# Optimization experiments

Hardware: AMD Instinct MI355X
Metric: run time of the kernel (lower is better)

## Reference

```python
import jax, jax.numpy as jnp
import numpy as np

MAX_POS = 512  # hardcoded max_pos_emb in the module
LN_EPS = 1e-5


def setup_inputs() -> dict:
    key = jax.random.key(0)
    ks = jax.random.split(key, 6)
    bs, n, d = 16, 4000, 1024
    h, dh = 8, 128
    inner = h * dh
    return {
        "x": jax.random.normal(ks[0], (bs, n, d), jnp.float32),
        "ln_w": jnp.ones((d,), jnp.float32),
        "ln_b": jnp.zeros((d,), jnp.float32),
        "Wq": (jax.random.normal(ks[1], (inner, d), jnp.float32) * 0.02),
        "Wkv": (jax.random.normal(ks[2], (2 * inner, d), jnp.float32) * 0.02),
        "Wo": (jax.random.normal(ks[3], (d, inner), jnp.float32) * 0.02),
        "bo": jnp.zeros((d,), jnp.float32),
        "rel_emb": (jax.random.normal(ks[4], (2 * MAX_POS + 1, dh), jnp.float32) * 0.02),
        "context_size": 256,
    }


def reference(x, ln_w, ln_b, Wq, Wkv, Wo, bo, rel_emb, context_size):
    bs, n, d = x.shape
    dh = rel_emb.shape[1]
    h = Wq.shape[0] // dh
    scale = dh ** -0.5
    cs = int(context_size)
    nb = -(-n // cs)          # ceil(n / cs)
    nr = n % cs

    # pre_norm (LayerNorm)
    mu = jnp.mean(x, axis=-1, keepdims=True)
    var = jnp.var(x, axis=-1, keepdims=True)
    xn = (x - mu) * jax.lax.rsqrt(var + LN_EPS) * ln_w + ln_b
    if nr > 0:
        xn = jnp.pad(xn, ((0, 0), (0, cs - nr), (0, 0)))

    q = xn @ Wq.T                    # (bs, nb*cs, h*dh)
    k, v = jnp.split(xn @ Wkv.T, 2, axis=-1)

    def blk(t):  # -> (bs, nb, h, cs, dh)
        return t.reshape(bs, nb, cs, h, dh).transpose(0, 1, 3, 2, 4)

    q, k, v = blk(q), blk(k), blk(v)

    # relative position bias, computed as a GEMM instead of broadcast-mul-sum
    seq = jnp.arange(cs)
    dist = jnp.clip(seq[:, None] - seq[None, :], -cs, cs) + MAX_POS
    rel = rel_emb[dist]                                     # (cs, cs, dh)
    pos_attn = jnp.einsum('bnhid,ijd->bnhij', q, rel) * scale

    if nr > 0:
        m = np.ones((cs, cs), dtype=bool)
        m[:nr, :nr] = False
        neg = -jnp.finfo(pos_attn.dtype).max
        pos_attn = pos_attn.at[:, -1].set(
            jnp.where(jnp.asarray(m), neg, pos_attn[:, -1]))

    # SDPA with additive mask: softmax(q k^T * scale + pos_attn) v
    scores = jnp.einsum('bnhid,bnhjd->bnhij', q, k) * scale + pos_attn
    attn = jax.nn.softmax(scores, axis=-1)
    out = jnp.einsum('bnhij,bnhjd->bnhid', attn, v)         # (bs, nb, h, cs, dh)

    out = out.transpose(0, 1, 3, 2, 4).reshape(bs, nb * cs, h * dh)[:, :n]
    return out @ Wo.T + bo  # dropout is identity in eval
```

## Files before the change

kernel.cpp:

```cpp
#include <hip/hip_runtime.h>

typedef __bf16 bf16;
typedef __bf16 bf16x8 __attribute__((ext_vector_type(8)));
typedef float f32x4 __attribute__((ext_vector_type(4)));

#define MFMA16(A,B,C) __builtin_amdgcn_mfma_f32_16x16x32_bf16(A,B,C,0,0,0)
#define SCALE 0.08838834764831843f
#define NEGBIG (-1e30f)

#define AS1(p) ((__attribute__((address_space(1))) void*)(p))
#define AS3(p) ((__attribute__((address_space(3))) void*)(p))

#define BAR() do { asm volatile("" ::: "memory"); __builtin_amdgcn_s_barrier(); asm volatile("" ::: "memory"); } while (0)

__global__ void cvt_bf16(const float* __restrict__ src, bf16* __restrict__ dst, int n) {
    int i = (blockIdx.x * 256 + threadIdx.x) * 4;
    if (i < n) {
        float4 v = *(const float4*)(src + i);
        dst[i + 0] = (bf16)v.x; dst[i + 1] = (bf16)v.y;
        dst[i + 2] = (bf16)v.z; dst[i + 3] = (bf16)v.w;
    }
}

__global__ __launch_bounds__(256) void ln_kernel(const float* __restrict__ x,
                                                 const float* __restrict__ w,
                                                 const float* __restrict__ b,
                                                 bf16* __restrict__ xn) {
    int row = blockIdx.x;
    int bb = row >> 12, p = row & 4095;
    int t = threadIdx.x;
    bf16* out = xn + ((size_t)row << 10);
    if (p >= 4000) {
        uint2 z; z.x = 0u; z.y = 0u;
        *(uint2*)(out + t * 4) = z;
        return;
    }
    float4 v = *(const float4*)(x + (((size_t)bb * 4000 + p) << 10) + t * 4);
    float s = v.x + v.y + v.z + v.w;
    float s2 = v.x * v.x + v.y * v.y + v.z * v.z + v.w * v.w;
#pragma unroll
    for (int m = 1; m < 64; m <<= 1) { s += __shfl_xor(s, m); s2 += __shfl_xor(s2, m); }
    __shared__ float red[8];
    int wv = t >> 6, l = t & 63;
    if (l == 0) { red[wv] = s; red[4 + wv] = s2; }
    __syncthreads();
    s = red[0] + red[1] + red[2] + red[3];
    s2 = red[4] + red[5] + red[6] + red[7];
    float mu = s * (1.f / 1024.f);
    float var = s2 * (1.f / 1024.f) - mu * mu;
    float inv = rsqrtf(var + 1e-5f);
    float4 wv4 = *(const float4*)(w + t * 4);
    float4 bv4 = *(const float4*)(b + t * 4);
    union { bf16 h[4]; uint2 u; } o;
    o.h[0] = (bf16)((v.x - mu) * inv * wv4.x + bv4.x);
    o.h[1] = (bf16)((v.y - mu) * inv * wv4.y + bv4.y);
    o.h[2] = (bf16)((v.z - mu) * inv * wv4.z + bv4.z);
    o.h[3] = (bf16)((v.w - mu) * inv * wv4.w + bv4.w);
    *(uint2*)(out + t * 4) = o.u;
}


__device__ __forceinline__ void stage_half(const bf16* __restrict__ src, int srow, int K,
                                           int kofs, bf16* ldsb, int w, int l) {
#pragma unroll
    for (int r = 0; r < 2; ++r) {
        int rh = (r * 8 + w) * 8 + (l >> 3);
        int chunk = (l & 7) ^ (rh & 7);
        __builtin_amdgcn_global_load_lds(AS1(src + (size_t)(srow + rh) * K + kofs + chunk * 8),
                                         AS3(ldsb + (r * 8 + w) * 512), 16, 0, 0);
    }
}

__device__ __forceinline__ bf16x8 fragLD(const bf16* base, int row, int ks, int lk) {
    int ch = ((ks * 4 + lk) ^ (row & 7)) * 8;
    return *(const bf16x8*)(base + row * 64 + ch);
}

#define RDA(AF, base, mofs) \
    _Pragma("unroll") for (int m = 0; m < 4; ++m) \
    _Pragma("unroll") for (int ks = 0; ks < 2; ++ks) \
        AF[m][ks] = fragLD(base, rA + (mofs + m) * 16 + lrow, ks, lk);

#define RDB2(nb, base) \
    _Pragma("unroll") for (int n = 0; n < 2; ++n) \
    _Pragma("unroll") for (int ks = 0; ks < 2; ++ks) \
        bfr[(nb) + n][ks] = fragLD(base, rB + ((nb) + n) * 16 + lrow, ks, lk);

#define MM(mb, AF, nb) do { \
    __builtin_amdgcn_s_setprio(1); \
    _Pragma("unroll") for (int m = 0; m < 4; ++m) \
    _Pragma("unroll") for (int n = 0; n < 2; ++n) \
    _Pragma("unroll") for (int ks = 0; ks < 2; ++ks) \
        acc[(mb) + m][(nb) + n] = MFMA16(AF[m][ks], bfr[(nb) + n][ks], acc[(mb) + m][(nb) + n]); \
    __builtin_amdgcn_s_setprio(0); } while (0)

template <int EPI>
__global__ __launch_bounds__(512, 2) void gemm256(const bf16* __restrict__ A,
                                                  const bf16* __restrict__ B,
                                                  bf16* __restrict__ C,
                                                  float* __restrict__ Cf,
                                                  const float* __restrict__ bias,
                                                  int M, int N, int K) {
    __shared__ __align__(16) bf16 LA[2 * 16384];
    __shared__ __align__(16) bf16 LB[2 * 16384];
    const int t = threadIdx.x;
    const int w = t >> 6, l = t & 63;
    const int lrow = l & 15, lk = l >> 4;
    const int wrM = w >> 2, wn = w & 3;
    const int rA = wrM * 128, rB = wn * 64;

    const int nwg = gridDim.x, cpx = nwg >> 3;
    const int swz = ((int)blockIdx.x & 7) * cpx + ((int)blockIdx.x >> 3);
    const int nbk = N >> 8;
    const int m0 = (swz / nbk) * 256;
    const int n0 = (swz % nbk) * 256;

    bf16* LA0 = LA;          bf16* LB0 = LB;
    bf16* LA1 = LA + 16384;  bf16* LB1 = LB + 16384;

    f32x4 acc[8][4] = {};
    bf16x8 afL[4][2], afH[4][2], bfr[4][2];

    const int NT = K >> 6, NI = K >> 7;

    stage_half(B, n0,       K, 0,  LB0,        w, l);
    stage_half(B, n0 + 128, K, 0,  LB0 + 8192, w, l);
    stage_half(A, m0,       K, 0,  LA0,        w, l);
    stage_half(A, m0 + 128, K, 0,  LA0 + 8192, w, l);
    stage_half(B, n0,       K, 64, LB1,        w, l);
    stage_half(B, n0 + 128, K, 64, LB1 + 8192, w, l);
    stage_half(A, m0,       K, 64, LA1,        w, l);
    asm volatile("s_waitcnt vmcnt(6)" ::: "memory");
    BAR();

    for (int i = 0; i < NI; ++i) {
        const int kS1 = (2 * i + 1) << 6;
        const int t2 = 2 * i + 2, t3 = 2 * i + 3;
        const int kS2 = ((t2 < NT) ? t2 : NT - 1) << 6;
        const int kS3 = ((t3 < NT) ? t3 : NT - 1) << 6;

        RDA(afL, LA0, 0);
        if (wn < 2) { RDB2(0, LB0); RDB2(2, LB0); } else { RDB2(0, LB0); }
        stage_half(A, m0 + 128, K, kS1, LA1 + 8192, w, l);
        BAR();
        MM(0, afL, 0);
        BAR();
        if (wn >= 2) { RDB2(2, LB0); }
        stage_half(B, n0, K, kS2, LB0, w, l);
        BAR();
        MM(0, afL, 2);
        BAR();
        RDA(afH, LA0, 4);
        stage_half(B, n0 + 128, K, kS2, LB0 + 8192, w, l);
        BAR();
        MM(4, afH, 0);
        BAR();
        stage_half(A, m0, K, kS2, LA0, w, l);
        BAR();
        MM(4, afH, 2);
        asm volatile("s_waitcnt vmcnt(6)" ::: "memory");
        BAR();
        RDA(afL, LA1, 0);
        if (wn < 2) { RDB2(0, LB1); RDB2(2, LB1); } else { RDB2(0, LB1); }
        stage_half(A, m0 + 128, K, kS2, LA0 + 8192, w, l);
        BAR();
        MM(0, afL, 0);
        BAR();
        if (wn >= 2) { RDB2(2, LB1); }
        stage_half(B, n0, K, kS3, LB1, w, l);
        BAR();
        MM(0, afL, 2);
        BAR();
        RDA(afH, LA1, 4);
        stage_half(B, n0 + 128, K, kS3, LB1 + 8192, w, l);
        BAR();
        MM(4, afH, 0);
        BAR();
        stage_half(A, m0, K, kS3, LA1, w, l);
        BAR();
        MM(4, afH, 2);
        asm volatile("s_waitcnt vmcnt(6)" ::: "memory");
        BAR();
    }

    asm volatile("s_waitcnt vmcnt(0)" ::: "memory");

    if (EPI == 0) {
#pragma unroll
        for (int m = 0; m < 8; ++m)
#pragma unroll
            for (int r = 0; r < 4; ++r) {
                size_t row = (size_t)(m0 + rA + m * 16 + lk * 4 + r);
                bf16* dst = C + row * N + n0 + rB;
#pragma unroll
                for (int n = 0; n < 4; ++n) dst[n * 16 + lrow] = (bf16)acc[m][n][r];
            }
    } else {
#pragma unroll
        for (int m = 0; m < 8; ++m)
#pragma unroll
            for (int r = 0; r < 4; ++r) {
                int row = m0 + rA + m * 16 + lk * 4 + r;
                int p = row & 4095, bb2 = row >> 12;
                if (p < 4000) {
                    float* dst = Cf + ((size_t)bb2 * 4000 + p) * 1024 + n0 + rB;
#pragma unroll
                    for (int n = 0; n < 4; ++n)
                        dst[n * 16 + lrow] = acc[m][n][r] + bias[n0 + rB + n * 16 + lrow];
                }
            }
    }
}

__global__ __launch_bounds__(512, 1) void attn_kernel(const bf16* __restrict__ qkv,
                                                      const bf16* __restrict__ relw,
                                                      bf16* __restrict__ ao) {
    int bb = blockIdx.x;
    int h = bb & 7, blkn = (bb >> 3) & 15, b = bb >> 7;
    const int t = threadIdx.x, w = t >> 6, l = t & 63, lrow = l & 15, lk = l >> 4;
    size_t qrow0 = (size_t)(b * 4096 + blkn * 256);
    __shared__ __align__(16) bf16 Vt[128 * 264];
    __shared__ __align__(16) bf16 Ps[8][16 * 72];

    const int i0 = w * 32;
    const bool last = (blkn == 15);
    const bf16* kbase = qkv + qrow0 * 3072 + 1024 + h * 128;

#pragma unroll
    for (int q = 0; q < 8; ++q) {
        int idx = q * 512 + t;
        int row = idx >> 4, c8 = idx & 15;
        bf16x8 vv = *(const bf16x8*)(qkv + (qrow0 + row) * 3072 + 2048 + h * 128 + c8 * 8);
        int jsw = row ^ ((c8 & 7) << 3);
#pragma unroll
        for (int e = 0; e < 8; ++e)
            Vt[(c8 * 8 + e) * 264 + jsw] = vv[e];
    }

    bf16x8 aq[2][4];
#pragma unroll
    for (int mt = 0; mt < 2; ++mt)
#pragma unroll
        for (int ks = 0; ks < 4; ++ks)
            aq[mt][ks] = *(const bf16x8*)(qkv + (qrow0 + i0 + mt * 16 + lrow) * 3072 +
                                          h * 128 + ks * 32 + lk * 8);

    f32x4 o[2][8] = {};
    float mrun[2][4], lrun[2][4];
#pragma unroll
    for (int mt = 0; mt < 2; ++mt)
#pragma unroll
        for (int r = 0; r < 4; ++r) { mrun[mt][r] = NEGBIG; lrun[mt][r] = 0.f; }

    __syncthreads();

    const int g0 = lk * 4 + 63 - lrow;
    bf16* ps = &Ps[w][0];

    for (int jt = 0; jt < 4; ++jt) {
        f32x4 s[2][4] = {};
        __builtin_amdgcn_s_setprio(1);
#pragma unroll
        for (int nt = 0; nt < 4; ++nt)
#pragma unroll
            for (int ks = 0; ks < 4; ++ks) {
                bf16x8 bk = *(const bf16x8*)(kbase +
                                (size_t)(jt * 64 + nt * 16 + lrow) * 3072 +
                                ks * 32 + lk * 8);
                s[0][nt] = MFMA16(aq[0][ks], bk, s[0][nt]);
                s[1][nt] = MFMA16(aq[1][ks], bk, s[1][nt]);
            }
        __builtin_amdgcn_s_setprio(0);

        const int cbase = i0 - jt * 64 + 192;
        f32x4 wacc[2][6] = {};
        __builtin_amdgcn_s_setprio(1);
#pragma unroll
        for (int ks = 0; ks < 4; ++ks)
#pragma unroll
            for (int ct = 0; ct < 6; ++ct) {
                bf16x8 br = *(const bf16x8*)(relw + (size_t)(cbase + ct * 16 + lrow) * 128 +
                                             ks * 32 + lk * 8);
                wacc[0][ct] = MFMA16(aq[0][ks], br, wacc[0][ct]);
                wacc[1][ct] = MFMA16(aq[1][ks], br, wacc[1][ct]);
            }
        __builtin_amdgcn_s_setprio(0);

#pragma unroll
        for (int mt = 0; mt < 2; ++mt)
#pragma unroll
            for (int r = 0; r < 4; ++r) {
                const int Kb = g0 + mt * 16 + r;
                const int dst = ((l & 48) | (Kb & 15)) << 2;
                unsigned pk[3];
#pragma unroll
                for (int P = 0; P < 3; ++P) {
                    unsigned lo = (unsigned)__builtin_bit_cast(unsigned short,
                                        (bf16)wacc[mt][2 * P][r]);
                    unsigned hi = (unsigned)__builtin_bit_cast(unsigned short,
                                        (bf16)wacc[mt][2 * P + 1][r]);
                    pk[P] = (unsigned)__builtin_amdgcn_ds_permute(dst, (int)((hi << 16) | lo));
                }
#pragma unroll
                for (int nt = 0; nt < 4; ++nt) {
                    int bcc = Kb - 16 * nt;
                    unsigned rec = (bcc < 32) ? pk[0] : (bcc < 64) ? pk[1] : pk[2];
                    unsigned b16v = ((bcc >> 4) & 1) ? (rec >> 16) : (rec & 0xffffu);
                    float wvf = __builtin_bit_cast(float, b16v << 16);
                    float xv = (s[mt][nt][r] + wvf) * SCALE;
                    if (last && (i0 + mt * 16 + lk * 4 + r >= 160 ||
                                 jt * 64 + nt * 16 + lrow >= 160))
                        xv = NEGBIG;
                    s[mt][nt][r] = xv;
                }
            }

#pragma unroll
        for (int mt = 0; mt < 2; ++mt)
#pragma unroll
            for (int r = 0; r < 4; ++r) {
                float mx = fmaxf(fmaxf(s[mt][0][r], s[mt][1][r]),
                                 fmaxf(s[mt][2][r], s[mt][3][r]));
#pragma unroll
                for (int d = 1; d < 16; d <<= 1) mx = fmaxf(mx, __shfl_xor(mx, d));
                float mold = mrun[mt][r];
                float mn = fmaxf(mold, mx);
                float corr = __expf(mold - mn);
                mrun[mt][r] = mn;
                float rs = 0.f;
#pragma unroll
                for (int nt = 0; nt < 4; ++nt) {
                    float e = __expf(s[mt][nt][r] - mn);
                    s[mt][nt][r] = e; rs += e;
                }
#pragma unroll
                for (int d = 1; d < 16; d <<= 1) rs += __shfl_xor(rs, d);
                lrun[mt][r] = lrun[mt][r] * corr + rs;
#pragma unroll
                for (int dt = 0; dt < 8; ++dt) o[mt][dt][r] *= corr;
            }

#pragma unroll
        for (int mt = 0; mt < 2; ++mt) {
#pragma unroll
            for (int nt = 0; nt < 4; ++nt)
#pragma unroll
                for (int r = 0; r < 4; ++r)
                    ps[(lk * 4 + r) * 72 + nt * 16 + lrow] = (bf16)s[mt][nt][r];
            __builtin_amdgcn_s_setprio(1);
#pragma unroll
            for (int pks = 0; pks < 2; ++pks) {
                bf16x8 ap = *(const bf16x8*)&ps[lrow * 72 + pks * 32 + lk * 8];
#pragma unroll
                for (int dt = 0; dt < 8; ++dt) {
                    int d = dt * 16 + lrow;
                    int jch = ((jt * 64 + pks * 32 + lk * 8) >> 3) ^ ((d >> 3) & 7);
                    bf16x8 bv = *(const bf16x8*)&Vt[d * 264 + (jch << 3)];
                    o[mt][dt] = MFMA16(ap, bv, o[mt][dt]);
                }
            }
            __builtin_amdgcn_s_setprio(0);
        }
    }

#pragma unroll
    for (int mt = 0; mt < 2; ++mt)
#pragma unroll
        for (int r = 0; r < 4; ++r) {
            float inv = 1.0f / lrun[mt][r];
            size_t arow = qrow0 + i0 + mt * 16 + lk * 4 + r;
            bf16* dst = ao + arow * 1024 + h * 128;
#pragma unroll
            for (int dt = 0; dt < 8; ++dt)
                dst[dt * 16 + lrow] = (bf16)(o[mt][dt][r] * inv);
        }
}

extern "C" void kernel_launch(void* const* d_in, const int* in_sizes, int n_in,
                              void* d_out, int out_size, void* d_ws, size_t ws_size,
                              hipStream_t stream) {
    const float* x   = (const float*)d_in[0];
    const float* lnw = (const float*)d_in[1];
    const float* lnb = (const float*)d_in[2];
    const float* Wq  = (const float*)d_in[3];
    const float* Wkv = (const float*)d_in[4];
    const float* Wo  = (const float*)d_in[5];
    const float* bo  = (const float*)d_in[6];
    const float* rel = (const float*)d_in[7];

    const size_t OFF_XN   = 0;
    const size_t OFF_QKV  = OFF_XN + 134217728ULL;
    const size_t OFF_WCAT = OFF_QKV + 402653184ULL;
    const size_t OFF_WO   = OFF_WCAT + 6291456ULL;
    const size_t OFF_RELW = OFF_WO + 2097152ULL;
    const size_t NEED     = OFF_RELW + 131072ULL;
    if (ws_size < NEED) return;

    char* ws = (char*)d_ws;
    bf16* xn   = (bf16*)(ws + OFF_XN);
    bf16* qkv  = (bf16*)(ws + OFF_QKV);
    bf16* wcat = (bf16*)(ws + OFF_WCAT);
    bf16* wo   = (bf16*)(ws + OFF_WO);
    bf16* relw = (bf16*)(ws + OFF_RELW);
    bf16* ao   = xn;
    float* out = (float*)d_out;

    cvt_bf16<<<1024, 256, 0, stream>>>(Wq, wcat, 1048576);
    cvt_bf16<<<2048, 256, 0, stream>>>(Wkv, wcat + 1048576, 2097152);
    cvt_bf16<<<1024, 256, 0, stream>>>(Wo, wo, 1048576);
    cvt_bf16<<<64, 256, 0, stream>>>(rel + 257 * 128, relw, 65536);
    ln_kernel<<<65536, 256, 0, stream>>>(x, lnw, lnb, xn);
    gemm256<0><<<3072, 512, 0, stream>>>(xn, wcat, qkv, nullptr, nullptr, 65536, 3072, 1024);
    attn_kernel<<<2048, 512, 0, stream>>>(qkv, relw, ao);
    gemm256<1><<<1024, 512, 0, stream>>>(ao, wo, nullptr, out, bo, 65536, 1024, 1024);
}
```

Measured before the change: 1.143 ms.

## Restructure attention to 16 waves with LDS-staged K/V tiles per key block

The attention kernel now uses 1024 threads with each wave owning 16 query rows instead of 32. K is staged in LDS 64 rows at a time rather than read per wave from global memory, and V is staged in a smaller per-tile transposed buffer. The next tile is loaded into registers before a barrier pair. The relative-position GEMM drops from 6 to 5 column tiles per wave because each wave covers fewer rows. This cuts redundant global K reads and LDS footprint but adds two block-wide barriers per key tile, and it halves the per-wave reuse of each B fragment.

```diff
diff --git a/kernel.cpp b/kernel.cpp
--- a/kernel.cpp
+++ b/kernel.cpp
@@ -212,45 +212,41 @@
     }
 }
 
-__global__ __launch_bounds__(512, 1) void attn_kernel(const bf16* __restrict__ qkv,
-                                                      const bf16* __restrict__ relw,
-                                                      bf16* __restrict__ ao) {
+__global__ __launch_bounds__(1024, 1) void attn_kernel(const bf16* __restrict__ qkv,
+                                                       const bf16* __restrict__ relw,
+                                                       bf16* __restrict__ ao) {
     int bb = blockIdx.x;
     int h = bb & 7, blkn = (bb >> 3) & 15, b = bb >> 7;
     const int t = threadIdx.x, w = t >> 6, l = t & 63, lrow = l & 15, lk = l >> 4;
     size_t qrow0 = (size_t)(b * 4096 + blkn * 256);
-    __shared__ __align__(16) bf16 Vt[128 * 264];
-    __shared__ __align__(16) bf16 Ps[8][16 * 72];
-
-    const int i0 = w * 32;
+    __shared__ __align__(16) bf16 Ks[64 * 136];
+    __shared__ __align__(16) bf16 Vt[128 * 72];
+    __shared__ __align__(16) bf16 Ps[16][16 * 72];
+
+    const int i0 = w * 16;
     const bool last = (blkn == 15);
-    const bf16* kbase = qkv + qrow0 * 3072 + 1024 + h * 128;
-
-#pragma unroll
-    for (int q = 0; q < 8; ++q) {
-        int idx = q * 512 + t;
-        int row = idx >> 4, c8 = idx & 15;
-        bf16x8 vv = *(const bf16x8*)(qkv + (qrow0 + row) * 3072 + 2048 + h * 128 + c8 * 8);
-        int jsw = row ^ ((c8 & 7) << 3);
+    const int srow = t >> 4, sc8 = t & 15;
+
+    {
+        bf16x8 kv = *(const bf16x8*)(qkv + (qrow0 + srow) * 3072 + 1024 + h * 128 + sc8 * 8);
+        *(bf16x8*)&Ks[srow * 136 + sc8 * 8] = kv;
+        bf16x8 vv = *(const bf16x8*)(qkv + (qrow0 + srow) * 3072 + 2048 + h * 128 + sc8 * 8);
+        int jsw = srow ^ ((sc8 & 7) << 3);
 #pragma unroll
         for (int e = 0; e < 8; ++e)
-            Vt[(c8 * 8 + e) * 264 + jsw] = vv[e];
-    }
-
-    bf16x8 aq[2][4];
-#pragma unroll
-    for (int mt = 0; mt < 2; ++mt)
-#pragma unroll
-        for (int ks = 0; ks < 4; ++ks)
-            aq[mt][ks] = *(const bf16x8*)(qkv + (qrow0 + i0 + mt * 16 + lrow) * 3072 +
-                                          h * 128 + ks * 32 + lk * 8);
-
-    f32x4 o[2][8] = {};
-    float mrun[2][4], lrun[2][4];
-#pragma unroll
-    for (int mt = 0; mt < 2; ++mt)
-#pragma unroll
-        for (int r = 0; r < 4; ++r) { mrun[mt][r] = NEGBIG; lrun[mt][r] = 0.f; }
+            Vt[(sc8 * 8 + e) * 72 + jsw] = vv[e];
+    }
+
+    bf16x8 aq[4];
+#pragma unroll
+    for (int ks = 0; ks < 4; ++ks)
+        aq[ks] = *(const bf16x8*)(qkv + (qrow0 + i0 + lrow) * 3072 +
+                                  h * 128 + ks * 32 + lk * 8);
+
+    f32x4 o[8] = {};
+    float mrun[4], lrun[4];
+#pragma unroll
+    for (int r = 0; r < 4; ++r) { mrun[r] = NEGBIG; lrun[r] = 0.f; }
 
     __syncthreads();
 
@@ -258,122 +254,126 @@
     bf16* ps = &Ps[w][0];
 
     for (int jt = 0; jt < 4; ++jt) {
-        f32x4 s[2][4] = {};
+        f32x4 s[4] = {};
         __builtin_amdgcn_s_setprio(1);
 #pragma unroll
         for (int nt = 0; nt < 4; ++nt)
 #pragma unroll
             for (int ks = 0; ks < 4; ++ks) {
-                bf16x8 bk = *(const bf16x8*)(kbase +
-                                (size_t)(jt * 64 + nt * 16 + lrow) * 3072 +
-                                ks * 32 + lk * 8);
-                s[0][nt] = MFMA16(aq[0][ks], bk, s[0][nt]);
-                s[1][nt] = MFMA16(aq[1][ks], bk, s[1][nt]);
+                bf16x8 bk = *(const bf16x8*)&Ks[(nt * 16 + lrow) * 136 + ks * 32 + lk * 8];
+                s[nt] = MFMA16(aq[ks], bk, s[nt]);
             }
         __builtin_amdgcn_s_setprio(0);
 
         const int cbase = i0 - jt * 64 + 192;
-        f32x4 wacc[2][6] = {};
+        f32x4 wacc[5] = {};
         __builtin_amdgcn_s_setprio(1);
 #pragma unroll
         for (int ks = 0; ks < 4; ++ks)
 #pragma unroll
-            for (int ct = 0; ct < 6; ++ct) {
+            for (int ct = 0; ct < 5; ++ct) {
                 bf16x8 br = *(const bf16x8*)(relw + (size_t)(cbase + ct * 16 + lrow) * 128 +
                                              ks * 32 + lk * 8);
-                wacc[0][ct] = MFMA16(aq[0][ks], br, wacc[0][ct]);
-                wacc[1][ct] = MFMA16(aq[1][ks], br, wacc[1][ct]);
+                wacc[ct] = MFMA16(aq[ks], br, wacc[ct]);
             }
         __builtin_amdgcn_s_setprio(0);
 
 #pragma unroll
-        for (int mt = 0; mt < 2; ++mt)
-#pragma unroll
-            for (int r = 0; r < 4; ++r) {
-                const int Kb = g0 + mt * 16 + r;
-                const int dst = ((l & 48) | (Kb & 15)) << 2;
-                unsigned pk[3];
-#pragma unroll
-                for (int P = 0; P < 3; ++P) {
-                    unsigned lo = (unsigned)__builtin_bit_cast(unsigned short,
-                                        (bf16)wacc[mt][2 * P][r]);
-                    unsigned hi = (unsigned)__builtin_bit_cast(unsigned short,
-                                        (bf16)wacc[mt][2 * P + 1][r]);
-                    pk[P] = (unsigned)__builtin_amdgcn_ds_permute(dst, (int)((hi << 16) | lo));
-                }
-#pragma unroll
-                for (int nt = 0; nt < 4; ++nt) {
-                    int bcc = Kb - 16 * nt;
-                    unsigned rec = (bcc < 32) ? pk[0] : (bcc < 64) ? pk[1] : pk[2];
-                    unsigned b16v = ((bcc >> 4) & 1) ? (rec >> 16) : (rec & 0xffffu);
-                    float wvf = __builtin_bit_cast(float, b16v << 16);
-                    float xv = (s[mt][nt][r] + wvf) * SCALE;
-                    if (last && (i0 + mt * 16 + lk * 4 + r >= 160 ||
-                                 jt * 64 + nt * 16 + lrow >= 160))
-                        xv = NEGBIG;
-                    s[mt][nt][r] = xv;
-                }
-            }
-
-#pragma unroll
-        for (int mt = 0; mt < 2; ++mt)
-#pragma unroll
-            for (int r = 0; r < 4; ++r) {
-                float mx = fmaxf(fmaxf(s[mt][0][r], s[mt][1][r]),
-                                 fmaxf(s[mt][2][r], s[mt][3][r]));
-#pragma unroll
-                for (int d = 1; d < 16; d <<= 1) mx = fmaxf(mx, __shfl_xor(mx, d));
-                float mold = mrun[mt][r];
-                float mn = fmaxf(mold, mx);
-                float corr = __expf(mold - mn);
-                mrun[mt][r] = mn;
-                float rs = 0.f;
-#pragma unroll
-                for (int nt = 0; nt < 4; ++nt) {
-                    float e = __expf(s[mt][nt][r] - mn);
-                    s[mt][nt][r] = e; rs += e;
-                }
-#pragma unroll
-                for (int d = 1; d < 16; d <<= 1) rs += __shfl_xor(rs, d);
-                lrun[mt][r] = lrun[mt][r] * corr + rs;
-#pragma unroll
-                for (int dt = 0; dt < 8; ++dt) o[mt][dt][r] *= corr;
-            }
-
-#pragma unroll
-        for (int mt = 0; mt < 2; ++mt) {
-#pragma unroll
-            for (int nt = 0; nt < 4; ++nt)
-#pragma unroll
-                for (int r = 0; r < 4; ++r)
-                    ps[(lk * 4 + r) * 72 + nt * 16 + lrow] = (bf16)s[mt][nt][r];
-            __builtin_amdgcn_s_setprio(1);
-#pragma unroll
-            for (int pks = 0; pks < 2; ++pks) {
-                bf16x8 ap = *(const bf16x8*)&ps[lrow * 72 + pks * 32 + lk * 8];
-#pragma unroll
-                for (int dt = 0; dt < 8; ++dt) {
-                    int d = dt * 16 + lrow;
-                    int jch = ((jt * 64 + pks * 32 + lk * 8) >> 3) ^ ((d >> 3) & 7);
-                    bf16x8 bv = *(const bf16x8*)&Vt[d * 264 + (jch << 3)];
-                    o[mt][dt] = MFMA16(ap, bv, o[mt][dt]);
-                }
-            }
-            __builtin_amdgcn_s_setprio(0);
+        for (int r = 0; r < 4; ++r) {
+            const int Kb = g0 + r;
+            const int dst = ((l & 48) | (Kb & 15)) << 2;
+            unsigned pk[3];
+#pragma unroll
+            for (int P = 0; P < 3; ++P) {
+                unsigned lo = (unsigned)__builtin_bit_cast(unsigned short,
+                                    (bf16)wacc[2 * P][r]);
+                unsigned hi = (2 * P + 1 < 5)
+                                  ? (unsigned)__builtin_bit_cast(unsigned short,
+                                        (bf16)wacc[2 * P + 1][r])
+                                  : 0u;
+                pk[P] = (unsigned)__builtin_amdgcn_ds_permute(dst, (int)((hi << 16) | lo));
+            }
+#pragma unroll
+            for (int nt = 0; nt < 4; ++nt) {
+                int bcc = Kb - 16 * nt;
+                unsigned rec = (bcc < 32) ? pk[0] : (bcc < 64) ? pk[1] : pk[2];
+                unsigned b16v = ((bcc >> 4) & 1) ? (rec >> 16) : (rec & 0xffffu);
+                float wvf = __builtin_bit_cast(float, b16v << 16);
+                float xv = (s[nt][r] + wvf) * SCALE;
+                if (last && (i0 + lk * 4 + r >= 160 ||
+                             jt * 64 + nt * 16 + lrow >= 160))
+                    xv = NEGBIG;
+                s[nt][r] = xv;
+            }
         }
-    }
-
-#pragma unroll
-    for (int mt = 0; mt < 2; ++mt)
+
 #pragma unroll
         for (int r = 0; r < 4; ++r) {
-            float inv = 1.0f / lrun[mt][r];
-            size_t arow = qrow0 + i0 + mt * 16 + lk * 4 + r;
-            bf16* dst = ao + arow * 1024 + h * 128;
-#pragma unroll
-            for (int dt = 0; dt < 8; ++dt)
-                dst[dt * 16 + lrow] = (bf16)(o[mt][dt][r] * inv);
+            float mx = fmaxf(fmaxf(s[0][r], s[1][r]), fmaxf(s[2][r], s[3][r]));
+#pragma unroll
+            for (int d = 1; d < 16; d <<= 1) mx = fmaxf(mx, __shfl_xor(mx, d));
+            float mold = mrun[r];
+            float mn = fmaxf(mold, mx);
+            float corr = __expf(mold - mn);
+            mrun[r] = mn;
+            float rs = 0.f;
+#pragma unroll
+            for (int nt = 0; nt < 4; ++nt) {
+                float e = __expf(s[nt][r] - mn);
+                s[nt][r] = e; rs += e;
+            }
+#pragma unroll
+            for (int d = 1; d < 16; d <<= 1) rs += __shfl_xor(rs, d);
+            lrun[r] = lrun[r] * corr + rs;
+#pragma unroll
+            for (int dt = 0; dt < 8; ++dt) o[dt][r] *= corr;
         }
+
+#pragma unroll
+        for (int nt = 0; nt < 4; ++nt)
+#pragma unroll
+            for (int r = 0; r < 4; ++r)
+                ps[(lk * 4 + r) * 72 + nt * 16 + lrow] = (bf16)s[nt][r];
+        __builtin_amdgcn_s_setprio(1);
+#pragma unroll
+        for (int pks = 0; pks < 2; ++pks) {
+            bf16x8 ap = *(const bf16x8*)&ps[lrow * 72 + pks * 32 + lk * 8];
+#pragma unroll
+            for (int dt = 0; dt < 8; ++dt) {
+                int d = dt * 16 + lrow;
+                int jx = (pks * 32 + lk * 8) ^ (((d >> 3) & 7) << 3);
+                bf16x8 bv = *(const bf16x8*)&Vt[d * 72 + jx];
+                o[dt] = MFMA16(ap, bv, o[dt]);
+            }
+        }
+        __builtin_amdgcn_s_setprio(0);
+
+        bf16x8 kreg, vreg;
+        if (jt < 3) {
+            int row = (jt + 1) * 64 + srow;
+            kreg = *(const bf16x8*)(qkv + (qrow0 + row) * 3072 + 1024 + h * 128 + sc8 * 8);
+            vreg = *(const bf16x8*)(qkv + (qrow0 + row) * 3072 + 2048 + h * 128 + sc8 * 8);
+        }
+        __syncthreads();
+        if (jt < 3) {
+            *(bf16x8*)&Ks[srow * 136 + sc8 * 8] = kreg;
+            int jsw = srow ^ ((sc8 & 7) << 3);
+#pragma unroll
+            for (int e = 0; e < 8; ++e)
+                Vt[(sc8 * 8 + e) * 72 + jsw] = vreg[e];
+        }
+        __syncthreads();
+    }
+
+#pragma unroll
+    for (int r = 0; r < 4; ++r) {
+        float inv = 1.0f / lrun[r];
+        size_t arow = qrow0 + i0 + lk * 4 + r;
+        bf16* dst = ao + arow * 1024 + h * 128;
+#pragma unroll
+        for (int dt = 0; dt < 8; ++dt)
+            dst[dt * 16 + lrow] = (bf16)(o[dt][r] * inv);
+    }
 }
 
 extern "C" void kernel_launch(void* const* d_in, const int* in_sizes, int n_in,
@@ -411,6 +411,6 @@
     cvt_bf16<<<64, 256, 0, stream>>>(rel + 257 * 128, relw, 65536);
     ln_kernel<<<65536, 256, 0, stream>>>(x, lnw, lnb, xn);
     gemm256<0><<<3072, 512, 0, stream>>>(xn, wcat, qkv, nullptr, nullptr, 65536, 3072, 1024);
-    attn_kernel<<<2048, 512, 0, stream>>>(qkv, relw, ao);
+    attn_kernel<<<2048, 1024, 0, stream>>>(qkv, relw, ao);
     gemm256<1><<<1024, 512, 0, stream>>>(ao, wo, nullptr, out, bo, 65536, 1024, 1024);
 }
```

Result: slower. 1.372 ms (+20.1%).
